# Performance work log

Hardware: AMD Instinct MI355X
Metric: run time of the kernel (lower is better)

## Reference

```python
import jax, jax.numpy as jnp
import numpy as np

N_NODES = 50000
N_EDGES = 800000
F_IN = 24
H = 128
N_GRAPHS = 100
BN_EPS = 1e-5


def setup_inputs() -> dict:
    key = jax.random.key(0)
    ks = jax.random.split(key, 12)
    x = jax.random.normal(ks[0], (N_NODES, F_IN), dtype=jnp.float32)
    edge_index = jax.random.randint(ks[1], (2, N_EDGES), 0, N_NODES, dtype=jnp.int32)
    batch = (jnp.arange(N_NODES, dtype=jnp.int32) // (N_NODES // N_GRAPHS)).astype(jnp.int32)

    def lin(k, fan_in, fan_out):
        bound = 1.0 / np.sqrt(fan_in)
        kw, kb = jax.random.split(k)
        W = jax.random.uniform(kw, (fan_in, fan_out), jnp.float32, -bound, bound)
        b = jax.random.uniform(kb, (fan_out,), jnp.float32, -bound, bound)
        return W, b

    W1, b1 = lin(ks[2], 2 * F_IN, H)
    W2, b2 = lin(ks[3], 2 * H, H)
    W3, b3 = lin(ks[4], 2 * H, H)
    Wl, bl = lin(ks[5], H, 1)
    g1 = jnp.ones((H,), jnp.float32); be1 = jnp.zeros((H,), jnp.float32)
    g2 = jnp.ones((H,), jnp.float32); be2 = jnp.zeros((H,), jnp.float32)
    g3 = jnp.ones((H,), jnp.float32); be3 = jnp.zeros((H,), jnp.float32)
    return {"x": x, "edge_index": edge_index, "batch": batch,
            "W1": W1, "b1": b1, "W2": W2, "b2": b2, "W3": W3, "b3": b3,
            "g1": g1, "be1": be1, "g2": g2, "be2": be2, "g3": g3, "be3": be3,
            "Wl": Wl, "bl": bl}


def edge_conv(x, src, dst, W, b):
    # PyG EdgeConv: message = mlp([x_i, x_j - x_i]) for edge j->i, aggr=max at i
    x_i = x[dst]                                    # [E, F]
    e = jnp.concatenate([x_i, x[src] - x_i], axis=-1)  # [E, 2F]
    m = jax.nn.relu(e @ W + b)                      # [E, H]
    out = jax.ops.segment_max(m, dst, num_segments=N_NODES)
    return jnp.where(jnp.isfinite(out), out, 0.0)   # isolated nodes -> 0


def batch_norm(h, g, b):
    # training-mode BN over node dim (biased variance), dropout treated as identity
    mu = h.mean(axis=0)
    var = ((h - mu) ** 2).mean(axis=0)
    return g * (h - mu) * jax.lax.rsqrt(var + BN_EPS) + b


def reference(x, edge_index, batch, W1, b1, W2, b2, W3, b3,
              g1, be1, g2, be2, g3, be3, Wl, bl):
    src, dst = edge_index[0], edge_index[1]
    h = edge_conv(x, src, dst, W1, b1)
    h = jax.nn.relu(batch_norm(h, g1, be1))
    h = edge_conv(h, src, dst, W2, b2)
    h = jax.nn.relu(batch_norm(h, g2, be2))
    h = edge_conv(h, src, dst, W3, b3)
    h = batch_norm(h, g3, be3)
    # global_mean_pool
    sums = jax.ops.segment_sum(h, batch, num_segments=N_GRAPHS)           # [G, H]
    counts = jax.ops.segment_sum(jnp.ones((h.shape[0],), h.dtype), batch,
                                 num_segments=N_GRAPHS)
    pooled = sums / jnp.maximum(counts, 1.0)[:, None]
    return jax.nn.relu(pooled @ Wl + bl)                                  # [G, 1]
```

## Files before the change

kernel.cpp:

```cpp
#include <hip/hip_runtime.h>

#define N_NODES 50000
#define N_EDGES 800000
#define F_IN 24
#define HDIM 128
#define N_GRAPHS 100
#define BN_EPS 1e-5f
#define NBLK 196
#define ROWS_PER_GRAPH (N_NODES / N_GRAPHS)
#define MM_GRID 782
#define HIST_BLKS ((N_EDGES + 255) / 256)
#define PREP_BLKS (F_IN + 2 * HDIM)
#define SSTR 32
#define SUMS_PER_LAYER (256 * SSTR)
#define STATS_BLKS 392
#define POOL_CHUNKS 10
#define POOL_BLKS (N_GRAPHS * POOL_CHUNKS)
#define ROWS_PER_CHUNK (ROWS_PER_GRAPH / POOL_CHUNKS)


typedef _Float16 h2 __attribute__((ext_vector_type(2)));
typedef _Float16 h4 __attribute__((ext_vector_type(4)));
typedef _Float16 f16x8 __attribute__((ext_vector_type(8)));
typedef float f32x4 __attribute__((ext_vector_type(4)));

template <int K, int KC>
__global__ __launch_bounds__(256) void k_mm1(const float* __restrict__ X,
                                             const float* __restrict__ Wcat,
                                             const float* __restrict__ bias,
                                             float* __restrict__ A, _Float16* __restrict__ C) {
    __shared__ float Xs[KC * 68];
    __shared__ float Ws[KC * 128];
    int tid = threadIdx.x;
    int row0 = blockIdx.x * 64;
    const bool isA = (blockIdx.y == 0);
    const int colbase = isA ? 0 : 128;
    int cg = tid & 31;
    int rg = tid >> 5;

    float acc[8][4];
#pragma unroll
    for (int ri = 0; ri < 8; ++ri)
#pragma unroll
        for (int ci = 0; ci < 4; ++ci)
            acc[ri][ci] = isA ? bias[cg * 4 + ci] : 0.f;

    for (int k0 = 0; k0 < K; k0 += KC) {
        __syncthreads();
        {
            const int C4 = KC / 4;
            for (int i = tid; i < 64 * C4; i += 256) {
                int c4 = i % C4, r = i / C4;
                int row = row0 + r;
                float4 v = make_float4(0.f, 0.f, 0.f, 0.f);
                if (row < N_NODES) v = *(const float4*)&X[row * K + k0 + c4 * 4];
                Xs[(c4 * 4 + 0) * 68 + r] = v.x;
                Xs[(c4 * 4 + 1) * 68 + r] = v.y;
                Xs[(c4 * 4 + 2) * 68 + r] = v.z;
                Xs[(c4 * 4 + 3) * 68 + r] = v.w;
            }
        }
        for (int i = tid; i < KC * 32; i += 256) {
            int c4 = i & 31, kr = i >> 5;
            *(float4*)&Ws[kr * 128 + c4 * 4] =
                *(const float4*)&Wcat[(k0 + kr) * 256 + colbase + c4 * 4];
        }
        __syncthreads();
#pragma unroll
        for (int kk = 0; kk < KC; ++kk) {
            float4 t0 = *(const float4*)&Xs[kk * 68 + rg * 8];
            float4 t1 = *(const float4*)&Xs[kk * 68 + rg * 8 + 4];
            float4 w = *(const float4*)&Ws[kk * 128 + cg * 4];
            float t[8] = {t0.x, t0.y, t0.z, t0.w, t1.x, t1.y, t1.z, t1.w};
            float wv[4] = {w.x, w.y, w.z, w.w};
#pragma unroll
            for (int ri = 0; ri < 8; ++ri)
#pragma unroll
                for (int ci = 0; ci < 4; ++ci)
                    acc[ri][ci] += t[ri] * wv[ci];
        }
    }

#pragma unroll
    for (int ri = 0; ri < 8; ++ri) {
        int row = row0 + rg * 8 + ri;
        if (row < N_NODES) {
            if (isA) {
                *(float4*)&A[row * HDIM + cg * 4] =
                    make_float4(acc[ri][0], acc[ri][1], acc[ri][2], acc[ri][3]);
            } else {
                union { h2 h[2]; uint2 u; } pk;
                pk.h[0] = h2{(_Float16)acc[ri][0], (_Float16)acc[ri][1]};
                pk.h[1] = h2{(_Float16)acc[ri][2], (_Float16)acc[ri][3]};
                *(uint2*)&C[row * HDIM + cg * 4] = pk.u;
            }
        }
    }
}

__global__ __launch_bounds__(256) void k_mmf(const _Float16* __restrict__ X,
                                             const _Float16* __restrict__ Wf,
                                             const float* __restrict__ bias,
                                             const float* __restrict__ sums,
                                             const float* __restrict__ g,
                                             const float* __restrict__ be,
                                             float* __restrict__ A, _Float16* __restrict__ C) {
    __shared__ _Float16 Xh[16 * 520];
    __shared__ _Float16 Wh[128 * 128];
    __shared__ float scs[128], shs[128];
    int tid = threadIdx.x;
    int lane = tid & 63, wv = tid >> 6;
    int row0 = blockIdx.x * 64;
    const bool isA = (blockIdx.y == 0);
    const _Float16* Wsrc = Wf + (isA ? 0 : 16384);

    if (tid < 128) {
        float S  = sums[tid * SSTR];
        float S2 = sums[(128 + tid) * SSTR];
        float mean = S / (float)N_NODES;
        float var = fmaxf(S2 / (float)N_NODES - mean * mean, 0.f);
        float scv = g[tid] / sqrtf(var + BN_EPS);
        scs[tid] = scv;
        shs[tid] = be[tid] - mean * scv;
    }
    {
        const uint4* s = (const uint4*)Wsrc;
        uint4* d = (uint4*)Wh;
        for (int i = tid; i < 2048; i += 256) d[i] = s[i];
    }
    __syncthreads();
    for (int i = tid; i < 64 * 32; i += 256) {
        int k4 = i & 31, rl = i >> 5;
        int row = row0 + rl;
        float4 v = make_float4(0.f, 0.f, 0.f, 0.f);
        if (row < N_NODES) {
            h4 xv = *(const h4*)&X[row * HDIM + k4 * 4];
            v = make_float4((float)xv.x, (float)xv.y, (float)xv.z, (float)xv.w);
        }
        int c = k4 * 4;
        v.x = fmaxf(v.x * scs[c + 0] + shs[c + 0], 0.f);
        v.y = fmaxf(v.y * scs[c + 1] + shs[c + 1], 0.f);
        v.z = fmaxf(v.z * scs[c + 2] + shs[c + 2], 0.f);
        v.w = fmaxf(v.w * scs[c + 3] + shs[c + 3], 0.f);
        int rt = rl >> 4, m = rl & 15, kc = k4 >> 3, q = (k4 >> 1) & 3, jh = k4 & 1;
        _Float16* d = Xh + (rt * 4 + kc) * 520 + (q * 16 + m) * 8 + jh * 4;
        d[0] = (_Float16)v.x; d[1] = (_Float16)v.y;
        d[2] = (_Float16)v.z; d[3] = (_Float16)v.w;
    }
    __syncthreads();

    int n = lane & 15, q = lane >> 4;
    f32x4 acc[8];
#pragma unroll
    for (int nt = 0; nt < 8; ++nt) {
        float b0 = isA ? bias[nt * 16 + n] : 0.f;
        acc[nt] = f32x4{b0, b0, b0, b0};
    }
#pragma unroll
    for (int kc = 0; kc < 4; ++kc) {
        f16x8 a = *(const f16x8*)(Xh + (wv * 4 + kc) * 520 + lane * 8);
#pragma unroll
        for (int nt = 0; nt < 8; ++nt) {
            f16x8 b = *(const f16x8*)(Wh + ((nt * 4 + kc) * 64 + lane) * 8);
            acc[nt] = __builtin_amdgcn_mfma_f32_16x16x32_f16(a, b, acc[nt], 0, 0, 0);
        }
    }
#pragma unroll
    for (int nt = 0; nt < 8; ++nt) {
#pragma unroll
        for (int r = 0; r < 4; ++r) {
            int row = row0 + wv * 16 + q * 4 + r;
            if (row < N_NODES) {
                int col = nt * 16 + n;
                if (isA) A[row * HDIM + col] = acc[nt][r];
                else     C[row * HDIM + col] = (_Float16)acc[nt][r];
            }
        }
    }
}

__global__ void k_pre(const float* __restrict__ W1, const float* __restrict__ W2,
                      const float* __restrict__ W3, float* __restrict__ Wcat1,
                      _Float16* __restrict__ Wf2, _Float16* __restrict__ Wf3,
                      const int* __restrict__ dst, unsigned* __restrict__ deg,
                      unsigned* __restrict__ rank) {
    int b = blockIdx.x;
    int j = threadIdx.x;
    if (b < F_IN) {
        float wb = W1[(b + F_IN) * HDIM + (j & 127)];
        float wt = W1[b * HDIM + (j & 127)];
        Wcat1[b * 256 + j] = (j < HDIM) ? (wt - wb) : wb;
    } else if (b < PREP_BLKS) {
        int idx = b - F_IN;
        int layer = idx >> 7;
        int k = idx & 127;
        const float* W = layer ? W3 : W2;
        _Float16* Wf   = layer ? Wf3 : Wf2;
        int col = j & 127;
        float wt = W[k * HDIM + col];
        float wb = W[(k + HDIM) * HDIM + col];
        float v = (j < 128) ? (wt - wb) : wb;
        int plane = j >> 7;
        int nt = col >> 4, n = col & 15, kc = k >> 5, q = (k >> 3) & 3, jj = k & 7;
        int f = ((nt * 4 + kc) * 4 + q) * 128 + n * 8 + jj;
        Wf[plane * 16384 + f] = (_Float16)v;
    } else {
        int e = (b - PREP_BLKS) * 256 + j;
        if (e < N_EDGES) rank[e] = atomicAdd(&deg[dst[e]], 1u);
    }
}

__global__ __launch_bounds__(256) void k_scanall(const unsigned* __restrict__ deg,
                                                 unsigned* __restrict__ bsum,
                                                 unsigned* __restrict__ off) {
    __shared__ unsigned s[256];
    int t = threadIdx.x;
    int b = blockIdx.x;
    int i = b * 256 + t;
    unsigned v = (i < N_NODES) ? deg[i] : 0u;
    s[t] = v;
    __syncthreads();
    for (int d = 1; d < 256; d <<= 1) {
        unsigned u = (t >= d) ? s[t - d] : 0u;
        __syncthreads();
        s[t] += u;
        __syncthreads();
    }
    unsigned locex = s[t] - v;
    if (t == 255) atomicExch(&bsum[b], s[255] + 1u);
    __syncthreads();
    unsigned bs = 0;
    if (t < NBLK) {
        unsigned x;
        do { x = atomicAdd(&bsum[t], 0u); } while (x == 0u);
        bs = x - 1u;
    }
    s[t] = (t < NBLK) ? bs : 0u;
    __syncthreads();
    for (int d = 1; d < 256; d <<= 1) {
        unsigned u = (t >= d) ? s[t - d] : 0u;
        __syncthreads();
        s[t] += u;
        __syncthreads();
    }
    unsigned bexcl = (b == 0) ? 0u : s[b - 1];
    if (i < N_NODES) off[i] = bexcl + locex;
}

__global__ void k_scatter(const int* __restrict__ src, const int* __restrict__ dst,
                          const unsigned* __restrict__ off, const unsigned* __restrict__ rank,
                          unsigned* __restrict__ ssrc) {
    int e = blockIdx.x * 256 + threadIdx.x;
    if (e < N_EDGES)
        ssrc[off[dst[e]] + rank[e]] = (unsigned)src[e];
}

__global__ __launch_bounds__(256) void k_agg(const float* __restrict__ A,
                                             const h2* __restrict__ Cc,
                                             const unsigned* __restrict__ off,
                                             const unsigned* __restrict__ deg,
                                             const unsigned* __restrict__ ssrc,
                                             h2* __restrict__ H) {
    __shared__ unsigned sl[4][64];
    int w = threadIdx.x >> 6;
    int lane = threadIdx.x & 63;
    int i = blockIdx.x * 4 + w;
    int d = (int)deg[i];
    unsigned o = off[i];
    union { unsigned short us[2]; h2 v; } ninf;
    ninf.us[0] = 0xFC00; ninf.us[1] = 0xFC00;
    h2 m2 = ninf.v;
    for (int base = 0; base < d; base += 64) {
        int cntc = min(64, d - base);
        if (lane < cntc) sl[w][lane] = ssrc[o + base + lane];
        int e = 0;
        for (; e + 8 <= cntc; e += 8) {
            unsigned s0 = sl[w][e + 0], s1 = sl[w][e + 1], s2 = sl[w][e + 2], s3 = sl[w][e + 3];
            unsigned s4 = sl[w][e + 4], s5 = sl[w][e + 5], s6 = sl[w][e + 6], s7 = sl[w][e + 7];
            h2 v0 = Cc[s0 * 64 + lane];
            h2 v1 = Cc[s1 * 64 + lane];
            h2 v2 = Cc[s2 * 64 + lane];
            h2 v3 = Cc[s3 * 64 + lane];
            h2 v4 = Cc[s4 * 64 + lane];
            h2 v5 = Cc[s5 * 64 + lane];
            h2 v6 = Cc[s6 * 64 + lane];
            h2 v7 = Cc[s7 * 64 + lane];
            h2 a0 = __builtin_elementwise_max(v0, v1);
            h2 a1 = __builtin_elementwise_max(v2, v3);
            h2 a2 = __builtin_elementwise_max(v4, v5);
            h2 a3 = __builtin_elementwise_max(v6, v7);
            h2 b0 = __builtin_elementwise_max(a0, a1);
            h2 b1 = __builtin_elementwise_max(a2, a3);
            m2 = __builtin_elementwise_max(m2, __builtin_elementwise_max(b0, b1));
        }
        if (e + 4 <= cntc) {
            unsigned s0 = sl[w][e + 0], s1 = sl[w][e + 1], s2 = sl[w][e + 2], s3 = sl[w][e + 3];
            h2 v0 = Cc[s0 * 64 + lane];
            h2 v1 = Cc[s1 * 64 + lane];
            h2 v2 = Cc[s2 * 64 + lane];
            h2 v3 = Cc[s3 * 64 + lane];
            h2 a0 = __builtin_elementwise_max(v0, v1);
            h2 a1 = __builtin_elementwise_max(v2, v3);
            m2 = __builtin_elementwise_max(m2, __builtin_elementwise_max(a0, a1));
            e += 4;
        }
        for (; e < cntc; ++e)
            m2 = __builtin_elementwise_max(m2, Cc[sl[w][e] * 64 + lane]);
    }
    float2 a = *(const float2*)&A[i * HDIM + lane * 2];
    float hx = (d > 0) ? fmaxf(a.x + (float)m2.x, 0.f) : 0.f;
    float hy = (d > 0) ? fmaxf(a.y + (float)m2.y, 0.f) : 0.f;
    H[i * 64 + lane] = h2{(_Float16)hx, (_Float16)hy};
}

__global__ __launch_bounds__(256) void k_stats(const _Float16* __restrict__ H,
                                               float* __restrict__ sums) {
    __shared__ float4 ls[256], ls2[256];
    int t = threadIdx.x;
    int c4 = t & 31, rg = t >> 5;
    int row0 = blockIdx.x * 128;
    float4 s = make_float4(0.f, 0.f, 0.f, 0.f);
    float4 s2 = make_float4(0.f, 0.f, 0.f, 0.f);
#pragma unroll 4
    for (int it = 0; it < 16; ++it) {
        int row = row0 + rg * 16 + it;
        if (row < N_NODES) {
            h4 hv = *(const h4*)&H[row * HDIM + c4 * 4];
            float4 v = make_float4((float)hv.x, (float)hv.y, (float)hv.z, (float)hv.w);
            s.x += v.x; s.y += v.y; s.z += v.z; s.w += v.w;
            s2.x += v.x * v.x; s2.y += v.y * v.y; s2.z += v.z * v.z; s2.w += v.w * v.w;
        }
    }
    ls[t] = s; ls2[t] = s2;
    __syncthreads();
    if (t < 32) {
        float4 a = ls[t], a2 = ls2[t];
#pragma unroll
        for (int j = 1; j < 8; ++j) {
            float4 b = ls[j * 32 + t], b2 = ls2[j * 32 + t];
            a.x += b.x; a.y += b.y; a.z += b.z; a.w += b.w;
            a2.x += b2.x; a2.y += b2.y; a2.z += b2.z; a2.w += b2.w;
        }
        int c = t * 4;
        atomicAdd(&sums[(c + 0) * SSTR], a.x);
        atomicAdd(&sums[(c + 1) * SSTR], a.y);
        atomicAdd(&sums[(c + 2) * SSTR], a.z);
        atomicAdd(&sums[(c + 3) * SSTR], a.w);
        atomicAdd(&sums[(128 + c + 0) * SSTR], a2.x);
        atomicAdd(&sums[(128 + c + 1) * SSTR], a2.y);
        atomicAdd(&sums[(128 + c + 2) * SSTR], a2.z);
        atomicAdd(&sums[(128 + c + 3) * SSTR], a2.w);
    }
}

__global__ __launch_bounds__(256) void k_pool2(const _Float16* __restrict__ H,
                                               float* __restrict__ Pp,
                                               float* __restrict__ sums) {
    __shared__ float4 ls[256], ls2[256];
    int t = threadIdx.x;
    int c4 = t & 31, rg = t >> 5;
    int b = blockIdx.x;
    int base = (b / POOL_CHUNKS) * ROWS_PER_GRAPH + (b % POOL_CHUNKS) * ROWS_PER_CHUNK;
    float4 s = make_float4(0.f, 0.f, 0.f, 0.f);
    float4 s2 = make_float4(0.f, 0.f, 0.f, 0.f);
#pragma unroll
    for (int j = 0; j < 7; ++j) {
        int rl = rg + j * 8;
        if (rl < ROWS_PER_CHUNK) {
            int row = base + rl;
            h4 hv = *(const h4*)&H[row * HDIM + c4 * 4];
            float4 v = make_float4((float)hv.x, (float)hv.y, (float)hv.z, (float)hv.w);
            s.x += v.x; s.y += v.y; s.z += v.z; s.w += v.w;
            s2.x += v.x * v.x; s2.y += v.y * v.y; s2.z += v.z * v.z; s2.w += v.w * v.w;
        }
    }
    ls[t] = s; ls2[t] = s2;
    __syncthreads();
    if (t < 32) {
        float4 a = ls[t], a2 = ls2[t];
#pragma unroll
        for (int j = 1; j < 8; ++j) {
            float4 q = ls[j * 32 + t], q2 = ls2[j * 32 + t];
            a.x += q.x; a.y += q.y; a.z += q.z; a.w += q.w;
            a2.x += q2.x; a2.y += q2.y; a2.z += q2.z; a2.w += q2.w;
        }
        int c = t * 4;
        *(float4*)&Pp[b * HDIM + c] = a;
        atomicAdd(&sums[(c + 0) * SSTR], a.x);
        atomicAdd(&sums[(c + 1) * SSTR], a.y);
        atomicAdd(&sums[(c + 2) * SSTR], a.z);
        atomicAdd(&sums[(c + 3) * SSTR], a.w);
        atomicAdd(&sums[(128 + c + 0) * SSTR], a2.x);
        atomicAdd(&sums[(128 + c + 1) * SSTR], a2.y);
        atomicAdd(&sums[(128 + c + 2) * SSTR], a2.z);
        atomicAdd(&sums[(128 + c + 3) * SSTR], a2.w);
    }
}

__global__ __launch_bounds__(128) void k_out(const float* __restrict__ Pp,
                                             const float* __restrict__ sums,
                                             const float* __restrict__ g3,
                                             const float* __restrict__ be3,
                                             const float* __restrict__ Wl,
                                             const float* __restrict__ bl,
                                             float* __restrict__ out) {
    int g = blockIdx.x;
    int k = threadIdx.x;
    float S  = sums[k * SSTR];
    float S2 = sums[(128 + k) * SSTR];
    float mean = S / (float)N_NODES;
    float var = fmaxf(S2 / (float)N_NODES - mean * mean, 0.f);
    float scv = g3[k] / sqrtf(var + BN_EPS);
    float shv = be3[k] - mean * scv;
    float pooled = 0.f;
#pragma unroll
    for (int j = 0; j < POOL_CHUNKS; ++j)
        pooled += Pp[(g * POOL_CHUNKS + j) * HDIM + k];
    float p = (scv * (pooled * (1.f / (float)ROWS_PER_GRAPH)) + shv) * Wl[k];
    __shared__ float red[2];
    for (int o = 32; o > 0; o >>= 1) p += __shfl_down(p, o);
    if ((k & 63) == 0) red[k >> 6] = p;
    __syncthreads();
    if (k == 0) out[g] = fmaxf(red[0] + red[1] + bl[0], 0.f);
}

extern "C" void kernel_launch(void* const* d_in, const int* in_sizes, int n_in,
                              void* d_out, int out_size, void* d_ws, size_t ws_size,
                              hipStream_t stream) {
    const float* x   = (const float*)d_in[0];
    const int* ei    = (const int*)d_in[1];
    const float* W1  = (const float*)d_in[3];
    const float* b1  = (const float*)d_in[4];
    const float* W2  = (const float*)d_in[5];
    const float* b2  = (const float*)d_in[6];
    const float* W3  = (const float*)d_in[7];
    const float* b3  = (const float*)d_in[8];
    const float* g1  = (const float*)d_in[9];
    const float* be1 = (const float*)d_in[10];
    const float* g2  = (const float*)d_in[11];
    const float* be2 = (const float*)d_in[12];
    const float* g3  = (const float*)d_in[13];
    const float* be3 = (const float*)d_in[14];
    const float* Wl  = (const float*)d_in[15];
    const float* bl  = (const float*)d_in[16];
    float* out = (float*)d_out;

    const int* srcp = ei;
    const int* dstp = ei + N_EDGES;

    char* ws = (char*)d_ws;
    size_t o = 0;
    auto alloc = [&](size_t bytes) -> void* {
        o = (o + 255) & ~(size_t)255;
        void* p = ws + o;
        o += bytes;
        return p;
    };
    float* A      = (float*)alloc((size_t)N_NODES * HDIM * 4);
    _Float16* C   = (_Float16*)alloc((size_t)N_NODES * HDIM * 2);
    _Float16* h   = (_Float16*)alloc((size_t)N_NODES * HDIM * 2);
    float* Wcat1  = (float*)alloc((size_t)F_IN * 256 * 4);
    _Float16* Wf2 = (_Float16*)alloc((size_t)2 * 16384 * 2);
    _Float16* Wf3 = (_Float16*)alloc((size_t)2 * 16384 * 2);
    unsigned* deg  = (unsigned*)alloc((size_t)N_NODES * 4);
    unsigned* bsum = (unsigned*)alloc((size_t)NBLK * 4);
    float* sums    = (float*)alloc((size_t)3 * SUMS_PER_LAYER * 4);
    unsigned* off  = (unsigned*)alloc((size_t)N_NODES * 4);
    unsigned* rank = (unsigned*)alloc((size_t)N_EDGES * 4);
    unsigned* ssrc = (unsigned*)alloc((size_t)N_EDGES * 4);
    float* Pp      = (float*)alloc((size_t)POOL_BLKS * HDIM * 4);
    (void)ws_size; (void)n_in; (void)in_sizes; (void)out_size;

    float* sums0 = sums;
    float* sums1 = sums + SUMS_PER_LAYER;
    float* sums2 = sums + 2 * SUMS_PER_LAYER;

    size_t zlen = (size_t)((char*)(sums + 3 * SUMS_PER_LAYER) - (char*)deg);
    (void)hipMemsetAsync(deg, 0, zlen, stream);

    k_pre<<<PREP_BLKS + HIST_BLKS, 256, 0, stream>>>(W1, W2, W3, Wcat1, Wf2, Wf3,
                                                     dstp, deg, rank);
    k_scanall<<<NBLK, 256, 0, stream>>>(deg, bsum, off);
    k_scatter<<<HIST_BLKS, 256, 0, stream>>>(srcp, dstp, off, rank, ssrc);

    const dim3 MMG(MM_GRID, 2);
    const int AGB = N_NODES / 4;

    k_mm1<F_IN, F_IN><<<MMG, 256, 0, stream>>>(x, Wcat1, b1, A, C);
    k_agg<<<AGB, 256, 0, stream>>>(A, (const h2*)C, off, deg, ssrc, (h2*)h);
    k_stats<<<STATS_BLKS, 256, 0, stream>>>(h, sums0);

    k_mmf<<<MMG, 256, 0, stream>>>(h, Wf2, b2, sums0, g1, be1, A, C);
    k_agg<<<AGB, 256, 0, stream>>>(A, (const h2*)C, off, deg, ssrc, (h2*)h);
    k_stats<<<STATS_BLKS, 256, 0, stream>>>(h, sums1);

    k_mmf<<<MMG, 256, 0, stream>>>(h, Wf3, b3, sums1, g2, be2, A, C);
    k_agg<<<AGB, 256, 0, stream>>>(A, (const h2*)C, off, deg, ssrc, (h2*)h);

    k_pool2<<<POOL_BLKS, 256, 0, stream>>>(h, Pp, sums2);
    k_out<<<N_GRAPHS, 128, 0, stream>>>(Pp, sums2, g3, be3, Wl, bl, out);
}
```

Measured before the change: 384.3 us.

## Compute both A and C halves per block in matmuls; deepen gather unroll in aggregation

```diff
diff --git a/kernel.cpp b/kernel.cpp
--- a/kernel.cpp
+++ b/kernel.cpp
@@ -30,20 +30,20 @@
                                              const float* __restrict__ bias,
                                              float* __restrict__ A, _Float16* __restrict__ C) {
     __shared__ float Xs[KC * 68];
-    __shared__ float Ws[KC * 128];
+    __shared__ float Ws[KC * 256];
     int tid = threadIdx.x;
     int row0 = blockIdx.x * 64;
-    const bool isA = (blockIdx.y == 0);
-    const int colbase = isA ? 0 : 128;
     int cg = tid & 31;
     int rg = tid >> 5;
 
-    float acc[8][4];
+    float accA[8][4], accC[8][4];
 #pragma unroll
     for (int ri = 0; ri < 8; ++ri)
 #pragma unroll
-        for (int ci = 0; ci < 4; ++ci)
-            acc[ri][ci] = isA ? bias[cg * 4 + ci] : 0.f;
+        for (int ci = 0; ci < 4; ++ci) {
+            accA[ri][ci] = bias[cg * 4 + ci];
+            accC[ri][ci] = 0.f;
+        }
 
     for (int k0 = 0; k0 < K; k0 += KC) {
         __syncthreads();
@@ -60,24 +60,28 @@
                 Xs[(c4 * 4 + 3) * 68 + r] = v.w;
             }
         }
-        for (int i = tid; i < KC * 32; i += 256) {
-            int c4 = i & 31, kr = i >> 5;
-            *(float4*)&Ws[kr * 128 + c4 * 4] =
-                *(const float4*)&Wcat[(k0 + kr) * 256 + colbase + c4 * 4];
+        for (int i = tid; i < KC * 64; i += 256) {
+            int c4 = i & 63, kr = i >> 6;
+            *(float4*)&Ws[kr * 256 + c4 * 4] =
+                *(const float4*)&Wcat[(k0 + kr) * 256 + c4 * 4];
         }
         __syncthreads();
 #pragma unroll
         for (int kk = 0; kk < KC; ++kk) {
             float4 t0 = *(const float4*)&Xs[kk * 68 + rg * 8];
             float4 t1 = *(const float4*)&Xs[kk * 68 + rg * 8 + 4];
-            float4 w = *(const float4*)&Ws[kk * 128 + cg * 4];
+            float4 wa = *(const float4*)&Ws[kk * 256 + cg * 4];
+            float4 wc = *(const float4*)&Ws[kk * 256 + 128 + cg * 4];
             float t[8] = {t0.x, t0.y, t0.z, t0.w, t1.x, t1.y, t1.z, t1.w};
-            float wv[4] = {w.x, w.y, w.z, w.w};
+            float wav[4] = {wa.x, wa.y, wa.z, wa.w};
+            float wcv[4] = {wc.x, wc.y, wc.z, wc.w};
 #pragma unroll
             for (int ri = 0; ri < 8; ++ri)
 #pragma unroll
-                for (int ci = 0; ci < 4; ++ci)
-                    acc[ri][ci] += t[ri] * wv[ci];
+                for (int ci = 0; ci < 4; ++ci) {
+                    accA[ri][ci] += t[ri] * wav[ci];
+                    accC[ri][ci] += t[ri] * wcv[ci];
+                }
         }
     }
 
@@ -85,15 +89,12 @@
     for (int ri = 0; ri < 8; ++ri) {
         int row = row0 + rg * 8 + ri;
         if (row < N_NODES) {
-            if (isA) {
-                *(float4*)&A[row * HDIM + cg * 4] =
-                    make_float4(acc[ri][0], acc[ri][1], acc[ri][2], acc[ri][3]);
-            } else {
-                union { h2 h[2]; uint2 u; } pk;
-                pk.h[0] = h2{(_Float16)acc[ri][0], (_Float16)acc[ri][1]};
-                pk.h[1] = h2{(_Float16)acc[ri][2], (_Float16)acc[ri][3]};
-                *(uint2*)&C[row * HDIM + cg * 4] = pk.u;
-            }
+            *(float4*)&A[row * HDIM + cg * 4] =
+                make_float4(accA[ri][0], accA[ri][1], accA[ri][2], accA[ri][3]);
+            union { h2 h[2]; uint2 u; } pk;
+            pk.h[0] = h2{(_Float16)accC[ri][0], (_Float16)accC[ri][1]};
+            pk.h[1] = h2{(_Float16)accC[ri][2], (_Float16)accC[ri][3]};
+            *(uint2*)&C[row * HDIM + cg * 4] = pk.u;
         }
     }
 }
@@ -111,8 +112,6 @@
     int tid = threadIdx.x;
     int lane = tid & 63, wv = tid >> 6;
     int row0 = blockIdx.x * 64;
-    const bool isA = (blockIdx.y == 0);
-    const _Float16* Wsrc = Wf + (isA ? 0 : 16384);
 
     if (tid < 128) {
         float S  = sums[tid * SSTR];
@@ -124,7 +123,7 @@
         shs[tid] = be[tid] - mean * scv;
     }
     {
-        const uint4* s = (const uint4*)Wsrc;
+        const uint4* s = (const uint4*)Wf;
         uint4* d = (uint4*)Wh;
         for (int i = tid; i < 2048; i += 256) d[i] = s[i];
     }
@@ -143,17 +142,18 @@
         v.z = fmaxf(v.z * scs[c + 2] + shs[c + 2], 0.f);
         v.w = fmaxf(v.w * scs[c + 3] + shs[c + 3], 0.f);
         int rt = rl >> 4, m = rl & 15, kc = k4 >> 3, q = (k4 >> 1) & 3, jh = k4 & 1;
-        _Float16* d = Xh + (rt * 4 + kc) * 520 + (q * 16 + m) * 8 + jh * 4;
-        d[0] = (_Float16)v.x; d[1] = (_Float16)v.y;
-        d[2] = (_Float16)v.z; d[3] = (_Float16)v.w;
+        _Float16* dp = Xh + (rt * 4 + kc) * 520 + (q * 16 + m) * 8 + jh * 4;
+        dp[0] = (_Float16)v.x; dp[1] = (_Float16)v.y;
+        dp[2] = (_Float16)v.z; dp[3] = (_Float16)v.w;
     }
     __syncthreads();
 
     int n = lane & 15, q = lane >> 4;
     f32x4 acc[8];
+
 #pragma unroll
     for (int nt = 0; nt < 8; ++nt) {
-        float b0 = isA ? bias[nt * 16 + n] : 0.f;
+        float b0 = bias[nt * 16 + n];
         acc[nt] = f32x4{b0, b0, b0, b0};
     }
 #pragma unroll
@@ -170,11 +170,34 @@
 #pragma unroll
         for (int r = 0; r < 4; ++r) {
             int row = row0 + wv * 16 + q * 4 + r;
-            if (row < N_NODES) {
-                int col = nt * 16 + n;
-                if (isA) A[row * HDIM + col] = acc[nt][r];
-                else     C[row * HDIM + col] = (_Float16)acc[nt][r];
-            }
+            if (row < N_NODES) A[row * HDIM + nt * 16 + n] = acc[nt][r];
+        }
+    }
+    __syncthreads();
+    {
+        const uint4* s = (const uint4*)(Wf + 16384);
+        uint4* d = (uint4*)Wh;
+        for (int i = tid; i < 2048; i += 256) d[i] = s[i];
+    }
+    __syncthreads();
+
+#pragma unroll
+    for (int nt = 0; nt < 8; ++nt) acc[nt] = f32x4{0.f, 0.f, 0.f, 0.f};
+#pragma unroll
+    for (int kc = 0; kc < 4; ++kc) {
+        f16x8 a = *(const f16x8*)(Xh + (wv * 4 + kc) * 520 + lane * 8);
+#pragma unroll
+        for (int nt = 0; nt < 8; ++nt) {
+            f16x8 b = *(const f16x8*)(Wh + ((nt * 4 + kc) * 64 + lane) * 8);
+            acc[nt] = __builtin_amdgcn_mfma_f32_16x16x32_f16(a, b, acc[nt], 0, 0, 0);
+        }
+    }
+#pragma unroll
+    for (int nt = 0; nt < 8; ++nt) {
+#pragma unroll
+        for (int r = 0; r < 4; ++r) {
+            int row = row0 + wv * 16 + q * 4 + r;
+            if (row < N_NODES) C[row * HDIM + nt * 16 + n] = (_Float16)acc[nt][r];
         }
     }
 }
@@ -267,47 +290,66 @@
     int i = blockIdx.x * 4 + w;
     int d = (int)deg[i];
     unsigned o = off[i];
+    float2 a = *(const float2*)&A[i * HDIM + lane * 2];
     union { unsigned short us[2]; h2 v; } ninf;
     ninf.us[0] = 0xFC00; ninf.us[1] = 0xFC00;
-    h2 m2 = ninf.v;
+    const h2 NI = ninf.v;
+    h2 m2 = NI;
     for (int base = 0; base < d; base += 64) {
         int cntc = min(64, d - base);
         if (lane < cntc) sl[w][lane] = ssrc[o + base + lane];
         int e = 0;
-        for (; e + 8 <= cntc; e += 8) {
-            unsigned s0 = sl[w][e + 0], s1 = sl[w][e + 1], s2 = sl[w][e + 2], s3 = sl[w][e + 3];
-            unsigned s4 = sl[w][e + 4], s5 = sl[w][e + 5], s6 = sl[w][e + 6], s7 = sl[w][e + 7];
-            h2 v0 = Cc[s0 * 64 + lane];
-            h2 v1 = Cc[s1 * 64 + lane];
-            h2 v2 = Cc[s2 * 64 + lane];
-            h2 v3 = Cc[s3 * 64 + lane];
-            h2 v4 = Cc[s4 * 64 + lane];
-            h2 v5 = Cc[s5 * 64 + lane];
-            h2 v6 = Cc[s6 * 64 + lane];
-            h2 v7 = Cc[s7 * 64 + lane];
-            h2 a0 = __builtin_elementwise_max(v0, v1);
-            h2 a1 = __builtin_elementwise_max(v2, v3);
-            h2 a2 = __builtin_elementwise_max(v4, v5);
-            h2 a3 = __builtin_elementwise_max(v6, v7);
-            h2 b0 = __builtin_elementwise_max(a0, a1);
-            h2 b1 = __builtin_elementwise_max(a2, a3);
-            m2 = __builtin_elementwise_max(m2, __builtin_elementwise_max(b0, b1));
-        }
-        if (e + 4 <= cntc) {
-            unsigned s0 = sl[w][e + 0], s1 = sl[w][e + 1], s2 = sl[w][e + 2], s3 = sl[w][e + 3];
-            h2 v0 = Cc[s0 * 64 + lane];
-            h2 v1 = Cc[s1 * 64 + lane];
-            h2 v2 = Cc[s2 * 64 + lane];
-            h2 v3 = Cc[s3 * 64 + lane];
-            h2 a0 = __builtin_elementwise_max(v0, v1);
-            h2 a1 = __builtin_elementwise_max(v2, v3);
-            m2 = __builtin_elementwise_max(m2, __builtin_elementwise_max(a0, a1));
-            e += 4;
-        }
-        for (; e < cntc; ++e)
-            m2 = __builtin_elementwise_max(m2, Cc[sl[w][e] * 64 + lane]);
-    }
-    float2 a = *(const float2*)&A[i * HDIM + lane * 2];
+        for (; e + 16 <= cntc; e += 16) {
+            unsigned s[16];
+#pragma unroll
+            for (int j = 0; j < 16; ++j) s[j] = sl[w][e + j];
+            h2 v[16];
+#pragma unroll
+            for (int j = 0; j < 16; ++j) v[j] = Cc[s[j] * 64 + lane];
+#pragma unroll
+            for (int st = 8; st > 0; st >>= 1)
+#pragma unroll
+                for (int j = 0; j < st; ++j)
+                    v[j] = __builtin_elementwise_max(v[j], v[j + st]);
+            m2 = __builtin_elementwise_max(m2, v[0]);
+        }
+        if (e + 8 <= cntc) {
+            unsigned s[8];
+#pragma unroll
+            for (int j = 0; j < 8; ++j) s[j] = sl[w][e + j];
+            h2 v[8];
+#pragma unroll
+            for (int j = 0; j < 8; ++j) v[j] = Cc[s[j] * 64 + lane];
+#pragma unroll
+            for (int st = 4; st > 0; st >>= 1)
+#pragma unroll
+                for (int j = 0; j < st; ++j)
+                    v[j] = __builtin_elementwise_max(v[j], v[j + st]);
+            m2 = __builtin_elementwise_max(m2, v[0]);
+            e += 8;
+        }
+        if (e < cntc) {
+            int last = cntc - 1;
+            unsigned s[8];
+#pragma unroll
+            for (int j = 0; j < 8; ++j) {
+                int idx = e + j;
+                s[j] = sl[w][idx < last ? idx : last];
+            }
+            h2 v[8];
+#pragma unroll
+            for (int j = 0; j < 8; ++j) v[j] = Cc[s[j] * 64 + lane];
+#pragma unroll
+            for (int j = 0; j < 8; ++j)
+                if (e + j >= cntc) v[j] = NI;
+#pragma unroll
+            for (int st = 4; st > 0; st >>= 1)
+#pragma unroll
+                for (int j = 0; j < st; ++j)
+                    v[j] = __builtin_elementwise_max(v[j], v[j + st]);
+            m2 = __builtin_elementwise_max(m2, v[0]);
+        }
+    }
     float hx = (d > 0) ? fmaxf(a.x + (float)m2.x, 0.f) : 0.f;
     float hy = (d > 0) ? fmaxf(a.y + (float)m2.y, 0.f) : 0.f;
     H[i * 64 + lane] = h2{(_Float16)hx, (_Float16)hy};
@@ -483,18 +525,17 @@
     k_scanall<<<NBLK, 256, 0, stream>>>(deg, bsum, off);
     k_scatter<<<HIST_BLKS, 256, 0, stream>>>(srcp, dstp, off, rank, ssrc);
 
-    const dim3 MMG(MM_GRID, 2);
     const int AGB = N_NODES / 4;
 
-    k_mm1<F_IN, F_IN><<<MMG, 256, 0, stream>>>(x, Wcat1, b1, A, C);
+    k_mm1<F_IN, F_IN><<<MM_GRID, 256, 0, stream>>>(x, Wcat1, b1, A, C);
     k_agg<<<AGB, 256, 0, stream>>>(A, (const h2*)C, off, deg, ssrc, (h2*)h);
     k_stats<<<STATS_BLKS, 256, 0, stream>>>(h, sums0);
 
-    k_mmf<<<MMG, 256, 0, stream>>>(h, Wf2, b2, sums0, g1, be1, A, C);
+    k_mmf<<<MM_GRID, 256, 0, stream>>>(h, Wf2, b2, sums0, g1, be1, A, C);
     k_agg<<<AGB, 256, 0, stream>>>(A, (const h2*)C, off, deg, ssrc, (h2*)h);
     k_stats<<<STATS_BLKS, 256, 0, stream>>>(h, sums1);
 
-    k_mmf<<<MMG, 256, 0, stream>>>(h, Wf3, b3, sums1, g2, be2, A, C);
+    k_mmf<<<MM_GRID, 256, 0, stream>>>(h, Wf3, b3, sums1, g2, be2, A, C);
     k_agg<<<AGB, 256, 0, stream>>>(A, (const h2*)C, off, deg, ssrc, (h2*)h);
 
     k_pool2<<<POOL_BLKS, 256, 0, stream>>>(h, Pp, sums2);
```

Measured after the change: 366.1 us. -4.7%, faster.
